# Kernel optimization log

Measured on AMD Instinct MI355X. Metric: run time of the kernel, lower is better.

## Reference

```python
import jax, jax.numpy as jnp
import numpy as np

NEG_SLOPE = 0.01  # torch nn.LeakyReLU default

def _lrelu(x):
    return jnp.where(x >= 0, x, NEG_SLOPE * x)

def setup_inputs() -> dict:
    key = jax.random.key(0)
    ks = jax.random.split(key, 10)
    B, Din, C = 128, 2048, 2048
    H = C // 2            # 1024
    OUT, KD = C // 4, 20  # 512, 20 (MBD)
    s = lambda k, shape, fan: jax.random.normal(k, shape, jnp.float32) / np.sqrt(fan)
    return {
        "inputs": jax.random.normal(ks[0], (B, Din), jnp.float32),
        "W1": s(ks[1], (Din, C), Din), "b1": jnp.zeros((C,), jnp.float32),
        "W2": s(ks[2], (C, H), C),     "b2": jnp.zeros((H,), jnp.float32),
        "W3": s(ks[3], (H, H), H),     "b3": jnp.zeros((H,), jnp.float32),
        "T":  jax.random.normal(ks[4], (H, OUT, KD), jnp.float32),
        "Wc": s(ks[5], (H + OUT, 1), H + OUT), "bc": jnp.zeros((1,), jnp.float32),
    }

def reference(inputs, W1, b1, W2, b2, W3, b3, T, Wc, bc):
    # dense stack: Linear + LeakyReLU x3
    h = _lrelu(inputs @ W1 + b1)          # [B, 2048]
    h = _lrelu(h @ W2 + b2)               # [B, 1024]
    h = _lrelu(h @ W3 + b3)               # [B, 1024]
    # minibatch discrimination
    Hd, OUT, KD = T.shape
    M = (h @ T.reshape(Hd, OUT * KD)).reshape(-1, OUT, KD)   # [B, OUT, KD]
    # pairwise L1 over kernel dim: [B, B, OUT]
    norm = jnp.abs(M[None, :, :, :] - M[:, None, :, :]).sum(-1)
    o_b = jnp.exp(-norm).sum(0) - 1.0     # [B, OUT] (subtract self-term)
    feat = jnp.concatenate([h, o_b], axis=1)  # [B, 1536]
    return feat @ Wc + bc                 # [B, 1]
```

## Files before the change

kernel.cpp:

```cpp
#include <hip/hip_runtime.h>
#include <hip/hip_bf16.h>


typedef __bf16 bf16x8 __attribute__((ext_vector_type(8)));
typedef float  f32x4  __attribute__((ext_vector_type(4)));

static __device__ __forceinline__ unsigned int f2bf(float f) {
  union { float f; unsigned int u; } v; v.f = f;
  unsigned int r = v.u + 0x7FFFu + ((v.u >> 16) & 1u);
  return r >> 16;
}
static __device__ __forceinline__ float bf2f(unsigned short u) {
  union { unsigned int u; float f; } v; v.u = ((unsigned int)u) << 16;
  return v.f;
}
static __device__ __forceinline__ float lrelu(float x) {
  return x >= 0.0f ? x : 0.01f * x;
}
static __device__ __forceinline__ void fma4(float4& c, float a, const float4& w) {
  c.x = fmaf(a, w.x, c.x); c.y = fmaf(a, w.y, c.y);
  c.z = fmaf(a, w.z, c.z); c.w = fmaf(a, w.w, c.w);
}

__global__ __launch_bounds__(256, 4) void gemm_f32(
    const float* __restrict__ A, const float* __restrict__ W,
    float* __restrict__ P, int lda, int N, int kchunk)
{
  __shared__ __align__(16) float As[16 * 128];
  __shared__ __align__(16) float Ws[16 * 32];
  const int t     = threadIdx.x;
  const int c0    = blockIdx.x * 32;
  const int kbase = blockIdx.y * kchunk;
  const int rowg  = t >> 3;
  const int colg  = t & 7;
  const int r_s   = t >> 1, kh_s = (t & 1) * 8;
  const int kw_s  = t >> 4, f_s  = (t & 15) * 2;

  float4 acc[4];
  acc[0] = make_float4(0, 0, 0, 0); acc[1] = make_float4(0, 0, 0, 0);
  acc[2] = make_float4(0, 0, 0, 0); acc[3] = make_float4(0, 0, 0, 0);

  const float* aptr = A + (size_t)r_s * lda + kbase + kh_s;
  const float* wptr = W + (size_t)(kbase + kw_s) * N + c0 + f_s;
  float4 pa0 = *(const float4*)aptr;
  float4 pa1 = *(const float4*)(aptr + 4);
  float2 pw  = *(const float2*)wptr;

  for (int kt = 0; kt < kchunk; kt += 16) {
    As[(kh_s + 0) * 128 + r_s] = pa0.x; As[(kh_s + 1) * 128 + r_s] = pa0.y;
    As[(kh_s + 2) * 128 + r_s] = pa0.z; As[(kh_s + 3) * 128 + r_s] = pa0.w;
    As[(kh_s + 4) * 128 + r_s] = pa1.x; As[(kh_s + 5) * 128 + r_s] = pa1.y;
    As[(kh_s + 6) * 128 + r_s] = pa1.z; As[(kh_s + 7) * 128 + r_s] = pa1.w;
    *(float2*)(Ws + kw_s * 32 + f_s) = pw;
    __syncthreads();
    if (kt + 16 < kchunk) {
      aptr += 16;
      wptr += (size_t)16 * N;
      pa0 = *(const float4*)aptr;
      pa1 = *(const float4*)(aptr + 4);
      pw  = *(const float2*)wptr;
    }
    #pragma unroll
    for (int k = 0; k < 16; k++) {
      float4 w = *(const float4*)(Ws + k * 32 + colg * 4);
      float4 a = *(const float4*)(As + k * 128 + rowg * 4);
      fma4(acc[0], a.x, w); fma4(acc[1], a.y, w);
      fma4(acc[2], a.z, w); fma4(acc[3], a.w, w);
    }
    __syncthreads();
  }

  float* op = P + (size_t)blockIdx.y * 128 * N + (size_t)(rowg * 4) * N + c0 + colg * 4;
  *(float4*)op           = acc[0];
  *(float4*)(op + N)     = acc[1];
  *(float4*)(op + 2 * N) = acc[2];
  *(float4*)(op + 3 * N) = acc[3];
}

__global__ __launch_bounds__(128) void reduce_ep(
    const float* __restrict__ P, const float* __restrict__ bias,
    float* __restrict__ outF, unsigned short* __restrict__ outB,
    int N, int S, int ldo)
{
  const int gid = blockIdx.x * 128 + threadIdx.x;
  const int c4  = N >> 2;
  const int r   = gid / c4;
  const int c   = (gid - r * c4) * 4;
  float4 s = make_float4(0, 0, 0, 0);
  for (int si = 0; si < S; si++) {
    float4 p = *(const float4*)(P + (size_t)si * 128 * N + (size_t)r * N + c);
    s.x += p.x; s.y += p.y; s.z += p.z; s.w += p.w;
  }
  float4 b = *(const float4*)(bias + c);
  s.x = lrelu(s.x + b.x); s.y = lrelu(s.y + b.y);
  s.z = lrelu(s.z + b.z); s.w = lrelu(s.w + b.w);
  *(float4*)(outF + (size_t)r * ldo + c) = s;
  if (outB) {
    ushort4 u;
    u.x = (unsigned short)f2bf(s.x); u.y = (unsigned short)f2bf(s.y);
    u.z = (unsigned short)f2bf(s.z); u.w = (unsigned short)f2bf(s.w);
    *(ushort4*)(outB + (size_t)r * N + c) = u;
  }
}

__global__ __launch_bounds__(256, 4) void gemm4_mfma(
    const unsigned short* __restrict__ h3b, const float* __restrict__ T,
    unsigned short* __restrict__ accM)
{
  __shared__ __align__(16) unsigned short Asm[128 * 40];
  __shared__ __align__(16) unsigned int   Wst[64 * 20];
  const int t     = threadIdx.x;
  const int c0    = blockIdx.x * 64;
  const int kbase = blockIdx.y * 256;
  const int lane  = t & 63, wave = t >> 6;
  const int ml    = lane & 15, q = lane >> 4;
  const int r0    = wave * 32;
  const int ra = t >> 2, qa = t & 3;
  const int kp = t & 15, n4 = (t >> 4) * 4;

  f32x4 acc[2][4];
  #pragma unroll
  for (int i = 0; i < 2; i++)
    #pragma unroll
    for (int j = 0; j < 4; j++) acc[i][j] = (f32x4){0.f, 0.f, 0.f, 0.f};

  const unsigned short* ap = h3b + (size_t)ra * 1024 + kbase + qa * 8;
  const float*          tp = T + (size_t)(kbase + 2 * kp) * 10240 + c0 + n4;
  uint4  va0 = *(const uint4*)ap;
  uint4  va1 = *(const uint4*)(ap + 64 * 1024);
  float4 vw0 = *(const float4*)tp;
  float4 vw1 = *(const float4*)(tp + 10240);

  for (int kt = 0; kt < 8; kt++) {
    *(uint4*)(Asm + ra * 40 + qa * 8)        = va0;
    *(uint4*)(Asm + (ra + 64) * 40 + qa * 8) = va1;
    Wst[(n4 + 0) * 20 + kp] = f2bf(vw0.x) | (f2bf(vw1.x) << 16);
    Wst[(n4 + 1) * 20 + kp] = f2bf(vw0.y) | (f2bf(vw1.y) << 16);
    Wst[(n4 + 2) * 20 + kp] = f2bf(vw0.z) | (f2bf(vw1.z) << 16);
    Wst[(n4 + 3) * 20 + kp] = f2bf(vw0.w) | (f2bf(vw1.w) << 16);
    __syncthreads();
    if (kt < 7) {
      ap += 32;
      tp += (size_t)32 * 10240;
      va0 = *(const uint4*)ap;
      va1 = *(const uint4*)(ap + 64 * 1024);
      vw0 = *(const float4*)tp;
      vw1 = *(const float4*)(tp + 10240);
    }
    bf16x8 a0 = *(const bf16x8*)(Asm + (r0 + ml) * 40 + q * 8);
    bf16x8 a1 = *(const bf16x8*)(Asm + (r0 + 16 + ml) * 40 + q * 8);
    #pragma unroll
    for (int ct = 0; ct < 4; ct++) {
      bf16x8 b = *(const bf16x8*)((const unsigned short*)Wst +
                                  (size_t)((ct * 16 + ml) * 20 + q * 4) * 2);
      acc[0][ct] = __builtin_amdgcn_mfma_f32_16x16x32_bf16(a0, b, acc[0][ct], 0, 0, 0);
      acc[1][ct] = __builtin_amdgcn_mfma_f32_16x16x32_bf16(a1, b, acc[1][ct], 0, 0, 0);
    }
    __syncthreads();
  }

  unsigned short* out = accM + (size_t)blockIdx.y * 128 * 10240;
  #pragma unroll
  for (int rt = 0; rt < 2; rt++)
    #pragma unroll
    for (int ct = 0; ct < 4; ct++) {
      int col = c0 + ct * 16 + ml;
      int row = r0 + rt * 16 + q * 4;
      #pragma unroll
      for (int i = 0; i < 4; i++)
        out[(size_t)(row + i) * 10240 + col] = (unsigned short)f2bf(acc[rt][ct][i]);
    }
}

__global__ __launch_bounds__(512, 4) void pairwise(
    const unsigned short* __restrict__ accM, float* __restrict__ feat)
{
  __shared__ __align__(16) float Ml[128 * 20];
  __shared__ float parts[8 * 128];
  const int t = threadIdx.x;
  const int o = blockIdx.x;
  {
    int i = t >> 2, kh = (t & 3) * 5;
    const unsigned short* p = accM + (size_t)i * 10240 + o * 20 + kh;
    #pragma unroll
    for (int k = 0; k < 5; k++) {
      float s = bf2f(p[k]) + bf2f(p[1310720 + k]) +
                bf2f(p[2621440 + k]) + bf2f(p[3932160 + k]);
      Ml[i * 20 + kh + k] = s;
    }
  }
  __syncthreads();

  const int jg = t & 63, ihalf = t >> 6;
  float mj[2][20];
  #pragma unroll
  for (int c = 0; c < 2; c++) {
    const float* src = Ml + (size_t)(jg * 2 + c) * 20;
    #pragma unroll
    for (int k = 0; k < 20; k++) mj[c][k] = src[k];
  }
  float acc[2] = {0.f, 0.f};
  for (int ii = 0; ii < 16; ii++) {
    int i = ihalf * 16 + ii;
    const float4* m4 = (const float4*)(Ml + (size_t)i * 20);
    float mi[20];
    *(float4*)(mi + 0)  = m4[0]; *(float4*)(mi + 4)  = m4[1];
    *(float4*)(mi + 8)  = m4[2]; *(float4*)(mi + 12) = m4[3];
    *(float4*)(mi + 16) = m4[4];
    #pragma unroll
    for (int c = 0; c < 2; c++) {
      float norm = 0.f;
      #pragma unroll
      for (int k = 0; k < 20; k++) norm += fabsf(mi[k] - mj[c][k]);
      acc[c] += __expf(-norm);
    }
  }
  #pragma unroll
  for (int c = 0; c < 2; c++) parts[ihalf * 128 + jg * 2 + c] = acc[c];
  __syncthreads();
  if (t < 128) {
    float s = 0.f;
    #pragma unroll
    for (int ih = 0; ih < 8; ih++) s += parts[ih * 128 + t];
    feat[(size_t)t * 1536 + 1024 + o] = s - 1.0f;
  }
}

__global__ __launch_bounds__(256) void final_dot(
    const float* __restrict__ feat, const float* __restrict__ Wc,
    const float* __restrict__ bc, float* __restrict__ out)
{
  __shared__ float red[4];
  const int t = threadIdx.x, r = blockIdx.x;
  float s = 0.f;
  for (int c = t; c < 1536; c += 256) s += feat[(size_t)r * 1536 + c] * Wc[c];
  for (int off = 32; off > 0; off >>= 1) s += __shfl_down(s, off);
  if ((t & 63) == 0) red[t >> 6] = s;
  __syncthreads();
  if (t == 0) out[r] = red[0] + red[1] + red[2] + red[3] + bc[0];
}

extern "C" void kernel_launch(void* const* d_in, const int* in_sizes, int n_in,
                              void* d_out, int out_size, void* d_ws, size_t ws_size,
                              hipStream_t stream)
{
  const float* X  = (const float*)d_in[0];
  const float* W1 = (const float*)d_in[1];
  const float* b1 = (const float*)d_in[2];
  const float* W2 = (const float*)d_in[3];
  const float* b2 = (const float*)d_in[4];
  const float* W3 = (const float*)d_in[5];
  const float* b3 = (const float*)d_in[6];
  const float* T  = (const float*)d_in[7];
  const float* Wc = (const float*)d_in[8];
  const float* bc = (const float*)d_in[9];

  char* ws = (char*)d_ws;
  float*          P    = (float*)ws;
  unsigned short* accB = (unsigned short*)ws;
  float*          h1   = (float*)(ws + 10485760);
  float*          h2   = (float*)(ws + 11534336);
  unsigned short* h3b  = (unsigned short*)(ws + 12058624);
  float*          feat = (float*)(ws + 12320768);
  float*          out  = (float*)d_out;

  gemm_f32<<<dim3(64, 8), 256, 0, stream>>>(X, W1, P, 2048, 2048, 256);
  reduce_ep<<<512, 128, 0, stream>>>(P, b1, h1, nullptr, 2048, 8, 2048);
  gemm_f32<<<dim3(32, 16), 256, 0, stream>>>(h1, W2, P, 2048, 1024, 128);
  reduce_ep<<<256, 128, 0, stream>>>(P, b2, h2, nullptr, 1024, 16, 1024);
  gemm_f32<<<dim3(32, 8), 256, 0, stream>>>(h2, W3, P, 1024, 1024, 128);
  reduce_ep<<<256, 128, 0, stream>>>(P, b3, feat, h3b, 1024, 8, 1536);
  gemm4_mfma<<<dim3(160, 4), 256, 0, stream>>>(h3b, T, accB);
  pairwise<<<512, 512, 0, stream>>>(accB, feat);
  final_dot<<<128, 256, 0, stream>>>(feat, Wc, bc, out);
}
```

Baseline: 194.6 us.

## Replace fp32 FMA dense GEMMs with split-bf16 three-term MFMA GEMMs

```diff
diff --git a/kernel.cpp b/kernel.cpp
--- a/kernel.cpp
+++ b/kernel.cpp
@@ -3,6 +3,7 @@
 
 
 typedef __bf16 bf16x8 __attribute__((ext_vector_type(8)));
+typedef __bf16 bf16x2 __attribute__((ext_vector_type(2)));
 typedef float  f32x4  __attribute__((ext_vector_type(4)));
 
 static __device__ __forceinline__ unsigned int f2bf(float f) {
@@ -14,73 +15,137 @@
   union { unsigned int u; float f; } v; v.u = ((unsigned int)u) << 16;
   return v.f;
 }
+static __device__ __forceinline__ unsigned int pack_bf16_rne(float a, float b) {
+  bf16x2 v; v[0] = (__bf16)a; v[1] = (__bf16)b;
+  return __builtin_bit_cast(unsigned int, v);
+}
 static __device__ __forceinline__ float lrelu(float x) {
   return x >= 0.0f ? x : 0.01f * x;
 }
-static __device__ __forceinline__ void fma4(float4& c, float a, const float4& w) {
-  c.x = fmaf(a, w.x, c.x); c.y = fmaf(a, w.y, c.y);
-  c.z = fmaf(a, w.z, c.z); c.w = fmaf(a, w.w, c.w);
-}
-
-__global__ __launch_bounds__(256, 4) void gemm_f32(
-    const float* __restrict__ A, const float* __restrict__ W,
-    float* __restrict__ P, int lda, int N, int kchunk)
-{
-  __shared__ __align__(16) float As[16 * 128];
-  __shared__ __align__(16) float Ws[16 * 32];
+
+__global__ __launch_bounds__(256) void convert_split(
+    const float* __restrict__ X, unsigned short* __restrict__ Hi,
+    unsigned short* __restrict__ Lo)
+{
+  const int g = blockIdx.x * 256 + threadIdx.x;
+  float a[8];
+  *(float4*)(a + 0) = *(const float4*)(X + (size_t)g * 8);
+  *(float4*)(a + 4) = *(const float4*)(X + (size_t)g * 8 + 4);
+  unsigned int hu[4], lu[4];
+  #pragma unroll
+  for (int i = 0; i < 4; i++) {
+    float x0 = a[2 * i], x1 = a[2 * i + 1];
+    unsigned int h = pack_bf16_rne(x0, x1);
+    float f0 = bf2f((unsigned short)(h & 0xFFFFu));
+    float f1 = bf2f((unsigned short)(h >> 16));
+    hu[i] = h;
+    lu[i] = pack_bf16_rne(x0 - f0, x1 - f1);
+  }
+  *(uint4*)(Hi + (size_t)g * 8) = *(uint4*)hu;
+  *(uint4*)(Lo + (size_t)g * 8) = *(uint4*)lu;
+}
+
+__global__ __launch_bounds__(256, 2) void gemm_mfma3(
+    const unsigned short* __restrict__ Ahi, const unsigned short* __restrict__ Alo,
+    const float* __restrict__ W, float* __restrict__ P,
+    int K, int N, int kchunk)
+{
+  __shared__ __align__(16) unsigned short AHs[128 * 40];
+  __shared__ __align__(16) unsigned short ALs[128 * 40];
+  __shared__ __align__(16) unsigned int   WHs[64 * 20];
+  __shared__ __align__(16) unsigned int   WLs[64 * 20];
   const int t     = threadIdx.x;
-  const int c0    = blockIdx.x * 32;
+  const int c0    = blockIdx.x * 64;
   const int kbase = blockIdx.y * kchunk;
-  const int rowg  = t >> 3;
-  const int colg  = t & 7;
-  const int r_s   = t >> 1, kh_s = (t & 1) * 8;
-  const int kw_s  = t >> 4, f_s  = (t & 15) * 2;
-
-  float4 acc[4];
-  acc[0] = make_float4(0, 0, 0, 0); acc[1] = make_float4(0, 0, 0, 0);
-  acc[2] = make_float4(0, 0, 0, 0); acc[3] = make_float4(0, 0, 0, 0);
-
-  const float* aptr = A + (size_t)r_s * lda + kbase + kh_s;
-  const float* wptr = W + (size_t)(kbase + kw_s) * N + c0 + f_s;
-  float4 pa0 = *(const float4*)aptr;
-  float4 pa1 = *(const float4*)(aptr + 4);
-  float2 pw  = *(const float2*)wptr;
-
-  for (int kt = 0; kt < kchunk; kt += 16) {
-    As[(kh_s + 0) * 128 + r_s] = pa0.x; As[(kh_s + 1) * 128 + r_s] = pa0.y;
-    As[(kh_s + 2) * 128 + r_s] = pa0.z; As[(kh_s + 3) * 128 + r_s] = pa0.w;
-    As[(kh_s + 4) * 128 + r_s] = pa1.x; As[(kh_s + 5) * 128 + r_s] = pa1.y;
-    As[(kh_s + 6) * 128 + r_s] = pa1.z; As[(kh_s + 7) * 128 + r_s] = pa1.w;
-    *(float2*)(Ws + kw_s * 32 + f_s) = pw;
+  const int lane  = t & 63, wave = t >> 6;
+  const int ml    = lane & 15, q = lane >> 4;
+  const int r0    = wave * 32;
+  const int ra = t >> 2, qa = t & 3;
+  const int kp = t & 15, n4 = (t >> 4) * 4;
+
+  f32x4 acc[2][4];
+  #pragma unroll
+  for (int i = 0; i < 2; i++)
+    #pragma unroll
+    for (int j = 0; j < 4; j++) acc[i][j] = (f32x4){0.f, 0.f, 0.f, 0.f};
+
+  const unsigned short* ahp = Ahi + (size_t)ra * K + kbase + qa * 8;
+  const unsigned short* alp = Alo + (size_t)ra * K + kbase + qa * 8;
+  const float*          wp  = W + (size_t)(kbase + 2 * kp) * N + c0 + n4;
+  uint4  vah0 = *(const uint4*)ahp;
+  uint4  vah1 = *(const uint4*)(ahp + (size_t)64 * K);
+  uint4  val0 = *(const uint4*)alp;
+  uint4  val1 = *(const uint4*)(alp + (size_t)64 * K);
+  float4 vw0 = *(const float4*)wp;
+  float4 vw1 = *(const float4*)(wp + N);
+
+  const int nkt = kchunk >> 5;
+  for (int kt = 0; kt < nkt; kt++) {
+    *(uint4*)(AHs + ra * 40 + qa * 8)        = vah0;
+    *(uint4*)(AHs + (ra + 64) * 40 + qa * 8) = vah1;
+    *(uint4*)(ALs + ra * 40 + qa * 8)        = val0;
+    *(uint4*)(ALs + (ra + 64) * 40 + qa * 8) = val1;
+    {
+      float w0[4], w1[4];
+      *(float4*)w0 = vw0; *(float4*)w1 = vw1;
+      #pragma unroll
+      for (int c = 0; c < 4; c++) {
+        unsigned int hu = pack_bf16_rne(w0[c], w1[c]);
+        float f0 = bf2f((unsigned short)(hu & 0xFFFFu));
+        float f1 = bf2f((unsigned short)(hu >> 16));
+        unsigned int lu = pack_bf16_rne(w0[c] - f0, w1[c] - f1);
+        WHs[(n4 + c) * 20 + kp] = hu;
+        WLs[(n4 + c) * 20 + kp] = lu;
+      }
+    }
     __syncthreads();
-    if (kt + 16 < kchunk) {
-      aptr += 16;
-      wptr += (size_t)16 * N;
-      pa0 = *(const float4*)aptr;
-      pa1 = *(const float4*)(aptr + 4);
-      pw  = *(const float2*)wptr;
-    }
-    #pragma unroll
-    for (int k = 0; k < 16; k++) {
-      float4 w = *(const float4*)(Ws + k * 32 + colg * 4);
-      float4 a = *(const float4*)(As + k * 128 + rowg * 4);
-      fma4(acc[0], a.x, w); fma4(acc[1], a.y, w);
-      fma4(acc[2], a.z, w); fma4(acc[3], a.w, w);
+    if (kt + 1 < nkt) {
+      ahp += 32; alp += 32;
+      wp  += (size_t)32 * N;
+      vah0 = *(const uint4*)ahp;
+      vah1 = *(const uint4*)(ahp + (size_t)64 * K);
+      val0 = *(const uint4*)alp;
+      val1 = *(const uint4*)(alp + (size_t)64 * K);
+      vw0 = *(const float4*)wp;
+      vw1 = *(const float4*)(wp + N);
+    }
+    bf16x8 ah0 = *(const bf16x8*)(AHs + (r0 + ml) * 40 + q * 8);
+    bf16x8 ah1 = *(const bf16x8*)(AHs + (r0 + 16 + ml) * 40 + q * 8);
+    bf16x8 al0 = *(const bf16x8*)(ALs + (r0 + ml) * 40 + q * 8);
+    bf16x8 al1 = *(const bf16x8*)(ALs + (r0 + 16 + ml) * 40 + q * 8);
+    #pragma unroll
+    for (int ct = 0; ct < 4; ct++) {
+      bf16x8 bh = *(const bf16x8*)((const unsigned short*)WHs +
+                                   (size_t)((ct * 16 + ml) * 20 + q * 4) * 2);
+      bf16x8 bl = *(const bf16x8*)((const unsigned short*)WLs +
+                                   (size_t)((ct * 16 + ml) * 20 + q * 4) * 2);
+      acc[0][ct] = __builtin_amdgcn_mfma_f32_16x16x32_bf16(ah0, bh, acc[0][ct], 0, 0, 0);
+      acc[1][ct] = __builtin_amdgcn_mfma_f32_16x16x32_bf16(ah1, bh, acc[1][ct], 0, 0, 0);
+      acc[0][ct] = __builtin_amdgcn_mfma_f32_16x16x32_bf16(ah0, bl, acc[0][ct], 0, 0, 0);
+      acc[1][ct] = __builtin_amdgcn_mfma_f32_16x16x32_bf16(ah1, bl, acc[1][ct], 0, 0, 0);
+      acc[0][ct] = __builtin_amdgcn_mfma_f32_16x16x32_bf16(al0, bh, acc[0][ct], 0, 0, 0);
+      acc[1][ct] = __builtin_amdgcn_mfma_f32_16x16x32_bf16(al1, bh, acc[1][ct], 0, 0, 0);
     }
     __syncthreads();
   }
 
-  float* op = P + (size_t)blockIdx.y * 128 * N + (size_t)(rowg * 4) * N + c0 + colg * 4;
-  *(float4*)op           = acc[0];
-  *(float4*)(op + N)     = acc[1];
-  *(float4*)(op + 2 * N) = acc[2];
-  *(float4*)(op + 3 * N) = acc[3];
+  float* op = P + (size_t)blockIdx.y * 128 * N;
+  #pragma unroll
+  for (int rt = 0; rt < 2; rt++)
+    #pragma unroll
+    for (int ct = 0; ct < 4; ct++) {
+      const int col = c0 + ct * 16 + ml;
+      const int row = r0 + rt * 16 + q * 4;
+      #pragma unroll
+      for (int i = 0; i < 4; i++)
+        op[(size_t)(row + i) * N + col] = acc[rt][ct][i];
+    }
 }
 
 __global__ __launch_bounds__(128) void reduce_ep(
     const float* __restrict__ P, const float* __restrict__ bias,
-    float* __restrict__ outF, unsigned short* __restrict__ outB,
-    int N, int S, int ldo)
+    float* __restrict__ outF, unsigned short* __restrict__ outHi,
+    unsigned short* __restrict__ outLo, int N, int S, int ldo)
 {
   const int gid = blockIdx.x * 128 + threadIdx.x;
   const int c4  = N >> 2;
@@ -94,12 +159,20 @@
   float4 b = *(const float4*)(bias + c);
   s.x = lrelu(s.x + b.x); s.y = lrelu(s.y + b.y);
   s.z = lrelu(s.z + b.z); s.w = lrelu(s.w + b.w);
-  *(float4*)(outF + (size_t)r * ldo + c) = s;
-  if (outB) {
-    ushort4 u;
-    u.x = (unsigned short)f2bf(s.x); u.y = (unsigned short)f2bf(s.y);
-    u.z = (unsigned short)f2bf(s.z); u.w = (unsigned short)f2bf(s.w);
-    *(ushort4*)(outB + (size_t)r * N + c) = u;
+  if (outF) *(float4*)(outF + (size_t)r * ldo + c) = s;
+  if (outHi) {
+    ushort4 uh;
+    uh.x = (unsigned short)f2bf(s.x); uh.y = (unsigned short)f2bf(s.y);
+    uh.z = (unsigned short)f2bf(s.z); uh.w = (unsigned short)f2bf(s.w);
+    *(ushort4*)(outHi + (size_t)r * N + c) = uh;
+    if (outLo) {
+      ushort4 ul;
+      ul.x = (unsigned short)f2bf(s.x - bf2f(uh.x));
+      ul.y = (unsigned short)f2bf(s.y - bf2f(uh.y));
+      ul.z = (unsigned short)f2bf(s.z - bf2f(uh.z));
+      ul.w = (unsigned short)f2bf(s.w - bf2f(uh.w));
+      *(ushort4*)(outLo + (size_t)r * N + c) = ul;
+    }
   }
 }
 
@@ -258,19 +331,24 @@
   char* ws = (char*)d_ws;
   float*          P    = (float*)ws;
   unsigned short* accB = (unsigned short*)ws;
-  float*          h1   = (float*)(ws + 10485760);
-  float*          h2   = (float*)(ws + 11534336);
-  unsigned short* h3b  = (unsigned short*)(ws + 12058624);
-  float*          feat = (float*)(ws + 12320768);
+  unsigned short* Xhi  = (unsigned short*)(ws + 10485760);
+  unsigned short* Xlo  = (unsigned short*)(ws + 11010048);
+  unsigned short* h1hi = (unsigned short*)(ws + 11534336);
+  unsigned short* h1lo = (unsigned short*)(ws + 12058624);
+  unsigned short* h2hi = (unsigned short*)(ws + 12582912);
+  unsigned short* h2lo = (unsigned short*)(ws + 12845056);
+  unsigned short* h3hi = (unsigned short*)(ws + 13107200);
+  float*          feat = (float*)(ws + 13369344);
   float*          out  = (float*)d_out;
 
-  gemm_f32<<<dim3(64, 8), 256, 0, stream>>>(X, W1, P, 2048, 2048, 256);
-  reduce_ep<<<512, 128, 0, stream>>>(P, b1, h1, nullptr, 2048, 8, 2048);
-  gemm_f32<<<dim3(32, 16), 256, 0, stream>>>(h1, W2, P, 2048, 1024, 128);
-  reduce_ep<<<256, 128, 0, stream>>>(P, b2, h2, nullptr, 1024, 16, 1024);
-  gemm_f32<<<dim3(32, 8), 256, 0, stream>>>(h2, W3, P, 1024, 1024, 128);
-  reduce_ep<<<256, 128, 0, stream>>>(P, b3, feat, h3b, 1024, 8, 1536);
-  gemm4_mfma<<<dim3(160, 4), 256, 0, stream>>>(h3b, T, accB);
+  convert_split<<<128, 256, 0, stream>>>(X, Xhi, Xlo);
+  gemm_mfma3<<<dim3(32, 8), 256, 0, stream>>>(Xhi, Xlo, W1, P, 2048, 2048, 256);
+  reduce_ep<<<512, 128, 0, stream>>>(P, b1, nullptr, h1hi, h1lo, 2048, 8, 0);
+  gemm_mfma3<<<dim3(16, 16), 256, 0, stream>>>(h1hi, h1lo, W2, P, 2048, 1024, 128);
+  reduce_ep<<<256, 128, 0, stream>>>(P, b2, nullptr, h2hi, h2lo, 1024, 16, 0);
+  gemm_mfma3<<<dim3(16, 8), 256, 0, stream>>>(h2hi, h2lo, W3, P, 1024, 1024, 128);
+  reduce_ep<<<256, 128, 0, stream>>>(P, b3, feat, h3hi, nullptr, 1024, 8, 1536);
+  gemm4_mfma<<<dim3(160, 4), 256, 0, stream>>>(h3hi, T, accB);
   pairwise<<<512, 512, 0, stream>>>(accB, feat);
   final_dot<<<128, 256, 0, stream>>>(feat, Wc, bc, out);
 }
```

Result: faster. 179.2 us (-7.9%).
